# Kernel optimization log

Measured on AMD Instinct MI355X. Metric: run time of the kernel, lower is better.

The kernel has to match this reference:

```python
import jax, jax.numpy as jnp
import numpy as np


def setup_inputs() -> dict:
    key = jax.random.key(0)
    ks = jax.random.split(key, 6)
    B, S, D, H = 8, 1024, 1024, 16
    dk = D // H
    inputs = jax.random.normal(ks[0], (B, S, D), dtype=jnp.float32)
    mask = jnp.ones((B, S), dtype=jnp.float32)
    scale = 0.02
    W_q = jax.random.normal(ks[1], (H, D, dk), dtype=jnp.float32) * scale
    W_k = jax.random.normal(ks[2], (H, D, dk), dtype=jnp.float32) * scale
    W_v = jax.random.normal(ks[3], (D, D), dtype=jnp.float32) * scale
    W_o = jax.random.normal(ks[4], (D, D), dtype=jnp.float32) * scale
    return {"inputs": inputs, "mask": mask, "W_q": W_q, "W_k": W_k,
            "W_v": W_v, "W_o": W_o}


def reference(inputs, mask, W_q, W_k, W_v, W_o):
    B, S, D = inputs.shape
    H, _, dk = W_q.shape
    # combined causal + padding mask: 1.0 where attention is disallowed
    causal = 1.0 - jnp.tril(jnp.ones((S, S), dtype=jnp.float32))  # [S,S]
    input_mask = mask[:, None, :] * mask[:, :, None]              # [B,S,S]
    bad = jnp.maximum(causal[None, :, :], 1.0 - input_mask)       # [B,S,S]

    V = jnp.einsum('bsd,de->bse', inputs, W_v)                    # shared values
    Q = jnp.einsum('bsd,hdk->bhsk', inputs, W_q)
    K = jnp.einsum('bsd,hdk->bhsk', inputs, W_k)
    scores = jnp.einsum('bhqk,bhsk->bhqs', Q, K) / jnp.sqrt(jnp.float32(dk))
    scores = scores - bad[:, None, :, :] * 1e9
    attn = jax.nn.softmax(scores, axis=-1)                        # [B,H,S,S]
    attn_avg = jnp.mean(attn, axis=1)                             # [B,S,S]
    Hout = jnp.einsum('bqs,bse->bqe', attn_avg, V)
    output = jnp.einsum('bqe,ed->bqd', Hout, W_o)
    return (output, attn_avg)
```

## Files before the change

kernel.cpp:

```cpp
#include <hip/hip_runtime.h>

typedef unsigned short ushort;
typedef __bf16 bf16x8 __attribute__((ext_vector_type(8)));
typedef float f32x4 __attribute__((ext_vector_type(4)));
typedef unsigned short us8v __attribute__((ext_vector_type(8)));

__device__ __forceinline__ ushort f2bf(float f) {
  unsigned u = __builtin_bit_cast(unsigned, f);
  u += 0x7FFFu + ((u >> 16) & 1u);
  return (ushort)(u >> 16);
}

__device__ __forceinline__ bf16x8 ld_bf16x8(const ushort* p) {
  uint4 v = *(const uint4*)p;
  return __builtin_bit_cast(bf16x8, v);
}

__device__ __forceinline__ void gl16(const ushort* g, ushort* l) {
  __builtin_amdgcn_global_load_lds(
      (const __attribute__((address_space(1))) void*)g,
      (__attribute__((address_space(3))) void*)l, 16, 0, 0);
}

__global__ __launch_bounds__(256) void pack_x(const float* __restrict__ in,
                                              ushort* __restrict__ out) {
  long i = (long)blockIdx.x * 256 + threadIdx.x;
  const float4* s = (const float4*)in;
  float4 a = s[i * 2], b = s[i * 2 + 1];
  us8v o;
  o[0] = f2bf(a.x); o[1] = f2bf(a.y); o[2] = f2bf(a.z); o[3] = f2bf(a.w);
  o[4] = f2bf(b.x); o[5] = f2bf(b.y); o[6] = f2bf(b.z); o[7] = f2bf(b.w);
  *(us8v*)&out[i * 8] = o;
}

__global__ __launch_bounds__(256) void transpose_pack(
    const float* __restrict__ src, ushort* __restrict__ dst,
    int sC, int dLd, long sBatch, long dBatch, float scale) {
  src += (long)blockIdx.z * sBatch;
  dst += (long)blockIdx.z * dBatch;
  const int r0 = blockIdx.y * 64, c0 = blockIdx.x * 64;
  __shared__ ushort T[64 * 68];
  const int t = threadIdx.x;
#pragma unroll
  for (int i = 0; i < 4; ++i) {
    int ch = t + 256 * i;
    int r = ch >> 4, c4 = ch & 15;
    float4 v = *(const float4*)&src[(long)(r0 + r) * sC + c0 + c4 * 4];
    T[(c4 * 4 + 0) * 68 + r] = f2bf(v.x * scale);
    T[(c4 * 4 + 1) * 68 + r] = f2bf(v.y * scale);
    T[(c4 * 4 + 2) * 68 + r] = f2bf(v.z * scale);
    T[(c4 * 4 + 3) * 68 + r] = f2bf(v.w * scale);
  }
  __syncthreads();
#pragma unroll
  for (int i = 0; i < 4; ++i) {
    int ch = t + 256 * i;
    int c = ch >> 4, r4 = ch & 15;
    ushort4 o;
    o.x = T[c * 68 + r4 * 4 + 0];
    o.y = T[c * 68 + r4 * 4 + 1];
    o.z = T[c * 68 + r4 * 4 + 2];
    o.w = T[c * 68 + r4 * 4 + 3];
    *(ushort4*)&dst[(long)(c0 + c) * dLd + r0 + r4 * 4] = o;
  }
}

template <int EPI, bool CAUSAL, int BN>
__global__ __launch_bounds__(512, 2) void gemmS(
    const ushort* __restrict__ A, const ushort* __restrict__ Bt,
    int N, int K, long aB, long bB,
    ushort* __restrict__ O_q, ushort* __restrict__ O_k, ushort* __restrict__ O_v,
    ushort* __restrict__ O_b, long oB,
    float* __restrict__ O_f) {
  constexpr int NC = BN / 64;
  __shared__ __align__(16) ushort As[256 * 64];
  __shared__ __align__(16) ushort Bs[BN * 64];
  const int tid = threadIdx.x;
  const int lane = tid & 63, w = tid >> 6;
  const int lr = lane & 15, lg = lane >> 4;

  const int nx = gridDim.x, ny = gridDim.y;
  long nwg = (long)nx * ny * gridDim.z;
  long hwid = blockIdx.x + (long)nx * (blockIdx.y + (long)ny * blockIdx.z);
  long cpx = nwg >> 3;
  long sid = (hwid & 7) * cpx + (hwid >> 3);
  int bx = (int)(sid % nx);
  int t2 = (int)(sid / nx);
  int by = t2 % ny, z = t2 / ny;

  const int row0 = by * 256, col0 = bx * BN;
  A += (long)z * aB;
  Bt += (long)z * bB;
  const int wrow = (w >> 2) * 128;
  const int wcol = (w & 3) * (BN / 4);

  f32x4 acc[8][NC] = {};
  const int kmax = CAUSAL ? (K < row0 + 256 ? K : row0 + 256) : K;
  const int nk = kmax >> 6;

  for (int kt = 0; kt < nk; ++kt) {
    const int k0 = kt << 6;
    __syncthreads();
#pragma unroll
    for (int j = 0; j < 4; ++j) {
      int c = tid + 512 * j;
      int r = c >> 3, c8 = (c & 7) ^ (r & 7);
      gl16(&A[(long)(row0 + r) * K + k0 + c8 * 8], &As[c * 8]);
    }
#pragma unroll
    for (int j = 0; j < NC; ++j) {
      int c = tid + 512 * j;
      int r = c >> 3, c8 = (c & 7) ^ (r & 7);
      gl16(&Bt[(long)(col0 + r) * K + k0 + c8 * 8], &Bs[c * 8]);
    }
    __syncthreads();
#pragma unroll
    for (int kk = 0; kk < 2; ++kk) {
      bf16x8 bfr[NC];
#pragma unroll
      for (int n = 0; n < NC; ++n) {
        int row = wcol + n * 16 + lr;
        int c8 = (kk * 4 + lg) ^ (row & 7);
        bfr[n] = ld_bf16x8(&Bs[row * 64 + c8 * 8]);
      }
#pragma unroll
      for (int m = 0; m < 8; ++m) {
        int row = wrow + m * 16 + lr;
        int c8 = (kk * 4 + lg) ^ (row & 7);
        bf16x8 af = ld_bf16x8(&As[row * 64 + c8 * 8]);
#pragma unroll
        for (int n = 0; n < NC; ++n)
          acc[m][n] = __builtin_amdgcn_mfma_f32_16x16x32_bf16(af, bfr[n], acc[m][n], 0, 0, 0);
      }
    }
  }

#pragma unroll
  for (int m = 0; m < 8; ++m)
#pragma unroll
    for (int n = 0; n < NC; ++n)
#pragma unroll
      for (int r = 0; r < 4; ++r) {
        int gr = row0 + wrow + m * 16 + lg * 4 + r;
        int gc = col0 + wcol + n * 16 + lr;
        float v = acc[m][n][r];
        if (EPI == 0) {
          int b = gr >> 10, s = gr & 1023;
          if (gc < 1024) {
            int h = gc >> 6, kq = gc & 63;
            O_q[(((long)(b * 16 + h) << 10) + s) * 64 + kq] = f2bf(v);
          } else if (gc < 2048) {
            int n2 = gc - 1024;
            int h = n2 >> 6, kq = n2 & 63;
            O_k[(((long)(b * 16 + h) << 10) + s) * 64 + kq] = f2bf(v);
          } else {
            int e = gc - 2048;
            O_v[((long)(b << 10) + e) * 1024 + s] = f2bf(v);
          }
        } else if (EPI == 1) {
          (O_b + (long)z * oB)[(long)gr * N + gc] = f2bf(v);
        } else {
          O_f[(long)gr * N + gc] = v;
        }
      }
}

__global__ __launch_bounds__(512, 2) void attn16(
    const ushort* __restrict__ Qb, const ushort* __restrict__ Kb,
    const float* __restrict__ mask, float* __restrict__ attn_out,
    ushort* __restrict__ attnb) {
  __shared__ __align__(16) ushort Ks[2][4 * 128 * 64];
  __shared__ float redS[2][8][16];
  const int tid = threadIdx.x;
  const int lane = tid & 63, w = tid >> 6;
  const int lr = lane & 15, lg = lane >> 4;
  const int hw = blockIdx.x + 32 * blockIdx.y;
  const int b = hw & 7;
  const int x2 = hw >> 3;
  const int q0a = x2 * 16;
  const int q0b = (63 - x2) * 16;
  const int NTb = ((63 - x2) >> 3) + 1;
  const int n1 = (NTb - 4) << 10;
  const int NTWa = (x2 >> 4) * 2 + 2;
  const int NTWb = ((63 - x2) >> 4) * 2 + 2;

  float mqa[4], mqb[4], ms[8];
#pragma unroll
  for (int r = 0; r < 4; ++r) {
    mqa[r] = mask[b * 1024 + q0a + lg * 4 + r];
    mqb[r] = mask[b * 1024 + q0b + lg * 4 + r];
  }
#pragma unroll
  for (int t = 0; t < 8; ++t) ms[t] = mask[b * 1024 + t * 128 + w * 16 + lr];

  auto stageG = [&](int buf, int t0, int nch, int h) {
    const long hb = ((long)(b * 16 + h)) << 10;
#pragma unroll 2
    for (int i = tid; i < nch; i += 512) {
      int j = i >> 10, r = (i >> 3) & 127, c8 = i & 7;
      gl16(&Kb[(hb + (t0 + j) * 128 + r) * 64 + ((c8 ^ (r & 7)) << 3)],
           &Ks[buf][i * 8]);
    }
  };

  const int row = w * 16 + lr;
  const int cs0 = ((0 + lg) ^ (row & 7)) * 8;
  const int cs1 = ((4 + lg) ^ (row & 7)) * 8;

  stageG(0, 0, 4096, 0);
  __syncthreads();

  f32x4 acca[4] = {};
  f32x4 accb[8] = {};
#pragma unroll 1
  for (int h = 0; h < 16; ++h) {
    const long hb = ((long)(b * 16 + h)) << 10;
    const bf16x8 qa0 = ld_bf16x8(&Qb[(hb + q0a + lr) * 64 + lg * 8]);
    const bf16x8 qa1 = ld_bf16x8(&Qb[(hb + q0a + lr) * 64 + 32 + lg * 8]);
    const bf16x8 qb0 = ld_bf16x8(&Qb[(hb + q0b + lr) * 64 + lg * 8]);
    const bf16x8 qb1 = ld_bf16x8(&Qb[(hb + q0b + lr) * 64 + 32 + lg * 8]);

    stageG(1, 4, n1, h);

    f32x4 sca[4], scb[8];
    float psa[4] = {0.f, 0.f, 0.f, 0.f}, psb[4] = {0.f, 0.f, 0.f, 0.f};
#pragma unroll
    for (int t = 0; t < 4; ++t) {
      const int sb = t * 128 + w * 16;
      const ushort* kr = &Ks[0][(t * 128 + row) * 64];
      bf16x8 k0 = ld_bf16x8(kr + cs0);
      bf16x8 k1 = ld_bf16x8(kr + cs1);
      {
        f32x4 d = {};
        d = __builtin_amdgcn_mfma_f32_16x16x32_bf16(qb0, k0, d, 0, 0, 0);
        d = __builtin_amdgcn_mfma_f32_16x16x32_bf16(qb1, k1, d, 0, 0, 0);
#pragma unroll
        for (int r = 0; r < 4; ++r) {
          float e = __expf(d[r]) * (mqb[r] * ms[t]);
          scb[t][r] = e;
          psb[r] += e;
        }
      }
      if (sb <= q0a) {
        f32x4 d = {};
        d = __builtin_amdgcn_mfma_f32_16x16x32_bf16(qa0, k0, d, 0, 0, 0);
        d = __builtin_amdgcn_mfma_f32_16x16x32_bf16(qa1, k1, d, 0, 0, 0);
#pragma unroll
        for (int r = 0; r < 4; ++r) {
          float e = __expf(d[r]) * (mqa[r] * ms[t]);
          if (sb == q0a) e = (lr <= lg * 4 + r) ? e : 0.f;
          sca[t][r] = e;
          psa[r] += e;
        }
      }
    }
    __syncthreads();

    if (h < 15) stageG(0, 0, 4096, h + 1);

#pragma unroll
    for (int t = 4; t < 8; ++t) {
      const int sb = t * 128 + w * 16;
      if (sb <= q0b) {
        const ushort* kr = &Ks[1][((t - 4) * 128 + row) * 64];
        bf16x8 k0 = ld_bf16x8(kr + cs0);
        bf16x8 k1 = ld_bf16x8(kr + cs1);
        f32x4 d = {};
        d = __builtin_amdgcn_mfma_f32_16x16x32_bf16(qb0, k0, d, 0, 0, 0);
        d = __builtin_amdgcn_mfma_f32_16x16x32_bf16(qb1, k1, d, 0, 0, 0);
#pragma unroll
        for (int r = 0; r < 4; ++r) {
          float e = __expf(d[r]) * (mqb[r] * ms[t]);
          if (sb == q0b) e = (lr <= lg * 4 + r) ? e : 0.f;
          scb[t][r] = e;
          psb[r] += e;
        }
      }
    }
#pragma unroll
    for (int r = 0; r < 4; ++r) {
      psa[r] += __shfl_xor(psa[r], 1);
      psa[r] += __shfl_xor(psa[r], 2);
      psa[r] += __shfl_xor(psa[r], 4);
      psa[r] += __shfl_xor(psa[r], 8);
      psb[r] += __shfl_xor(psb[r], 1);
      psb[r] += __shfl_xor(psb[r], 2);
      psb[r] += __shfl_xor(psb[r], 4);
      psb[r] += __shfl_xor(psb[r], 8);
    }
    if (lr == 0) {
#pragma unroll
      for (int r = 0; r < 4; ++r) {
        redS[0][w][lg * 4 + r] = psa[r];
        redS[1][w][lg * 4 + r] = psb[r];
      }
    }
    __syncthreads();

#pragma unroll
    for (int r = 0; r < 4; ++r) {
      float ta = 0.f, tb = 0.f;
#pragma unroll
      for (int ww = 0; ww < 8; ++ww) {
        ta += redS[0][ww][lg * 4 + r];
        tb += redS[1][ww][lg * 4 + r];
      }
      float ra = __builtin_amdgcn_rcpf(ta);
      float rb = __builtin_amdgcn_rcpf(tb);
#pragma unroll
      for (int t = 0; t < 4; ++t) {
        const int sb = t * 128 + w * 16;
        if (sb <= q0a) acca[t][r] += sca[t][r] * ra;
      }
#pragma unroll
      for (int t = 0; t < 8; ++t) {
        const int sb = t * 128 + w * 16;
        if (sb <= q0b) accb[t][r] += scb[t][r] * rb;
      }
    }
  }

#pragma unroll
  for (int t = 0; t < 8; ++t) {
    int s = t * 128 + w * 16 + lr;
#pragma unroll
    for (int r = 0; r < 4; ++r) {
      {
        int q = q0a + lg * 4 + r;
        float v = (t < 4 ? acca[t][r] : 0.f) * 0.0625f;
        long o = ((long)(b * 1024 + q) << 10) + s;
        attn_out[o] = v;
        if (t < NTWa) attnb[o] = f2bf(v);
      }
      {
        int q = q0b + lg * 4 + r;
        float v = accb[t][r] * 0.0625f;
        long o = ((long)(b * 1024 + q) << 10) + s;
        attn_out[o] = v;
        if (t < NTWb) attnb[o] = f2bf(v);
      }
    }
  }
}

extern "C" void kernel_launch(void* const* d_in, const int* in_sizes, int n_in,
                              void* d_out, int out_size, void* d_ws, size_t ws_size,
                              hipStream_t stream) {
  const float* inputs = (const float*)d_in[0];
  const float* mask   = (const float*)d_in[1];
  const float* W_q    = (const float*)d_in[2];
  const float* W_k    = (const float*)d_in[3];
  const float* W_v    = (const float*)d_in[4];
  const float* W_o    = (const float*)d_in[5];
  float* out = (float*)d_out;

  ushort* Xb    = (ushort*)d_ws;
  ushort* WqkvT = Xb + 8192L * 1024;
  ushort* WoT   = WqkvT + 3072L * 1024;
  ushort* Qb    = WoT + 1024L * 1024;
  ushort* Kb    = Qb + 8L * 16 * 1024 * 64;
  ushort* Vt    = Kb + 8L * 16 * 1024 * 64;
  ushort* attnb = Vt + 8L * 1024 * 1024;
  ushort* Houtb = attnb + 8L * 1024 * 1024;

  pack_x<<<4096, 256, 0, stream>>>(inputs, Xb);
  transpose_pack<<<dim3(1, 16, 16), 256, 0, stream>>>(W_q, WqkvT, 64, 1024,
                                                      65536L, 64L * 1024, 0.125f);
  transpose_pack<<<dim3(1, 16, 16), 256, 0, stream>>>(W_k, WqkvT + 1024L * 1024, 64, 1024,
                                                      65536L, 64L * 1024, 1.0f);
  transpose_pack<<<dim3(16, 16, 1), 256, 0, stream>>>(W_v, WqkvT + 2048L * 1024, 1024, 1024,
                                                      0L, 0L, 1.0f);
  transpose_pack<<<dim3(16, 16, 1), 256, 0, stream>>>(W_o, WoT, 1024, 1024,
                                                      0L, 0L, 1.0f);
  gemmS<0, false, 192><<<dim3(16, 32, 1), 512, 0, stream>>>(
      Xb, WqkvT, 3072, 1024, 0L, 0L, Qb, Kb, Vt, nullptr, 0L, nullptr);
  attn16<<<dim3(32, 8), 512, 0, stream>>>(Qb, Kb, mask, out + 8388608L, attnb);
  gemmS<1, true, 128><<<dim3(8, 4, 8), 512, 0, stream>>>(
      attnb, Vt, 1024, 1024, 1048576L, 1048576L,
      nullptr, nullptr, nullptr, Houtb, 1048576L, nullptr);
  gemmS<2, false, 128><<<dim3(8, 32, 1), 512, 0, stream>>>(
      Houtb, WoT, 1024, 1024, 0L, 0L,
      nullptr, nullptr, nullptr, nullptr, 0L, out);
}
```

Baseline: 250.5 us.

## Switch GEMMs to 128x128 tiles with 256 threads and trim causal padding

Replaces the 256xBN, 512-thread GEMM with a 128x128-tile, 256-thread kernel. It uses a 2x2 wave layout with 4x4 MFMA fragments per wave and allows 3 blocks per CU. A template flag selects which grid index (rows or columns) varies fastest in the block-to-tile mapping. Because the causal attn@V GEMM now reads K only up to row0+128, attn16 writes fewer padding tiles, which cuts extra stores. The trade is more blocks and better load balance against less data reuse per tile, so global/LDS traffic per FLOP goes up.

```diff
diff --git a/kernel.cpp b/kernel.cpp
--- a/kernel.cpp
+++ b/kernel.cpp
@@ -65,16 +65,15 @@
   }
 }
 
-template <int EPI, bool CAUSAL, int BN>
-__global__ __launch_bounds__(512, 2) void gemmS(
+template <int EPI, bool CAUSAL, int SWZ>
+__global__ __launch_bounds__(256, 3) void gemm4(
     const ushort* __restrict__ A, const ushort* __restrict__ Bt,
     int N, int K, long aB, long bB,
     ushort* __restrict__ O_q, ushort* __restrict__ O_k, ushort* __restrict__ O_v,
     ushort* __restrict__ O_b, long oB,
     float* __restrict__ O_f) {
-  constexpr int NC = BN / 64;
-  __shared__ __align__(16) ushort As[256 * 64];
-  __shared__ __align__(16) ushort Bs[BN * 64];
+  __shared__ __align__(16) ushort As[128 * 64];
+  __shared__ __align__(16) ushort Bs[128 * 64];
   const int tid = threadIdx.x;
   const int lane = tid & 63, w = tid >> 6;
   const int lr = lane & 15, lg = lane >> 4;
@@ -84,18 +83,26 @@
   long hwid = blockIdx.x + (long)nx * (blockIdx.y + (long)ny * blockIdx.z);
   long cpx = nwg >> 3;
   long sid = (hwid & 7) * cpx + (hwid >> 3);
-  int bx = (int)(sid % nx);
-  int t2 = (int)(sid / nx);
-  int by = t2 % ny, z = t2 / ny;
-
-  const int row0 = by * 256, col0 = bx * BN;
+  int bx, by, z;
+  if (SWZ == 1) {
+    by = (int)(sid % ny);
+    int t2 = (int)(sid / ny);
+    bx = t2 % nx;
+    z = t2 / nx;
+  } else {
+    bx = (int)(sid % nx);
+    int t2 = (int)(sid / nx);
+    by = t2 % ny;
+    z = t2 / ny;
+  }
+
+  const int row0 = by * 128, col0 = bx * 128;
   A += (long)z * aB;
   Bt += (long)z * bB;
-  const int wrow = (w >> 2) * 128;
-  const int wcol = (w & 3) * (BN / 4);
-
-  f32x4 acc[8][NC] = {};
-  const int kmax = CAUSAL ? (K < row0 + 256 ? K : row0 + 256) : K;
+  const int wr = (w >> 1) * 64, wc = (w & 1) * 64;
+
+  f32x4 acc[4][4] = {};
+  const int kmax = CAUSAL ? (K < row0 + 128 ? K : row0 + 128) : K;
   const int nk = kmax >> 6;
 
   for (int kt = 0; kt < nk; ++kt) {
@@ -103,46 +110,43 @@
     __syncthreads();
 #pragma unroll
     for (int j = 0; j < 4; ++j) {
-      int c = tid + 512 * j;
+      int c = tid + 256 * j;
       int r = c >> 3, c8 = (c & 7) ^ (r & 7);
       gl16(&A[(long)(row0 + r) * K + k0 + c8 * 8], &As[c * 8]);
-    }
-#pragma unroll
-    for (int j = 0; j < NC; ++j) {
-      int c = tid + 512 * j;
-      int r = c >> 3, c8 = (c & 7) ^ (r & 7);
       gl16(&Bt[(long)(col0 + r) * K + k0 + c8 * 8], &Bs[c * 8]);
     }
     __syncthreads();
 #pragma unroll
     for (int kk = 0; kk < 2; ++kk) {
-      bf16x8 bfr[NC];
-#pragma unroll
-      for (int n = 0; n < NC; ++n) {
-        int row = wcol + n * 16 + lr;
+      bf16x8 af[4], bfr[4];
+#pragma unroll
+      for (int m = 0; m < 4; ++m) {
+        int row = wr + m * 16 + lr;
+        int c8 = (kk * 4 + lg) ^ (row & 7);
+        af[m] = ld_bf16x8(&As[row * 64 + c8 * 8]);
+      }
+#pragma unroll
+      for (int n = 0; n < 4; ++n) {
+        int row = wc + n * 16 + lr;
         int c8 = (kk * 4 + lg) ^ (row & 7);
         bfr[n] = ld_bf16x8(&Bs[row * 64 + c8 * 8]);
       }
 #pragma unroll
-      for (int m = 0; m < 8; ++m) {
-        int row = wrow + m * 16 + lr;
-        int c8 = (kk * 4 + lg) ^ (row & 7);
-        bf16x8 af = ld_bf16x8(&As[row * 64 + c8 * 8]);
-#pragma unroll
-        for (int n = 0; n < NC; ++n)
-          acc[m][n] = __builtin_amdgcn_mfma_f32_16x16x32_bf16(af, bfr[n], acc[m][n], 0, 0, 0);
-      }
-    }
-  }
-
-#pragma unroll
-  for (int m = 0; m < 8; ++m)
-#pragma unroll
-    for (int n = 0; n < NC; ++n)
+      for (int m = 0; m < 4; ++m)
+#pragma unroll
+        for (int n = 0; n < 4; ++n)
+          acc[m][n] = __builtin_amdgcn_mfma_f32_16x16x32_bf16(af[m], bfr[n], acc[m][n], 0, 0, 0);
+    }
+  }
+
+#pragma unroll
+  for (int m = 0; m < 4; ++m)
+#pragma unroll
+    for (int n = 0; n < 4; ++n)
 #pragma unroll
       for (int r = 0; r < 4; ++r) {
-        int gr = row0 + wrow + m * 16 + lg * 4 + r;
-        int gc = col0 + wcol + n * 16 + lr;
+        int gr = row0 + wr + m * 16 + lg * 4 + r;
+        int gc = col0 + wc + n * 16 + lr;
         float v = acc[m][n][r];
         if (EPI == 0) {
           int b = gr >> 10, s = gr & 1023;
@@ -181,8 +185,8 @@
   const int q0b = (63 - x2) * 16;
   const int NTb = ((63 - x2) >> 3) + 1;
   const int n1 = (NTb - 4) << 10;
-  const int NTWa = (x2 >> 4) * 2 + 2;
-  const int NTWb = ((63 - x2) >> 4) * 2 + 2;
+  const int NTWa = (x2 >> 3) + 1;
+  const int NTWb = ((63 - x2) >> 3) + 1;
 
   float mqa[4], mqb[4], ms[8];
 #pragma unroll
@@ -372,13 +376,13 @@
                                                       0L, 0L, 1.0f);
   transpose_pack<<<dim3(16, 16, 1), 256, 0, stream>>>(W_o, WoT, 1024, 1024,
                                                       0L, 0L, 1.0f);
-  gemmS<0, false, 192><<<dim3(16, 32, 1), 512, 0, stream>>>(
+  gemm4<0, false, 1><<<dim3(24, 64, 1), 256, 0, stream>>>(
       Xb, WqkvT, 3072, 1024, 0L, 0L, Qb, Kb, Vt, nullptr, 0L, nullptr);
   attn16<<<dim3(32, 8), 512, 0, stream>>>(Qb, Kb, mask, out + 8388608L, attnb);
-  gemmS<1, true, 128><<<dim3(8, 4, 8), 512, 0, stream>>>(
+  gemm4<1, true, 0><<<dim3(8, 8, 8), 256, 0, stream>>>(
       attnb, Vt, 1024, 1024, 1048576L, 1048576L,
       nullptr, nullptr, nullptr, Houtb, 1048576L, nullptr);
-  gemmS<2, false, 128><<<dim3(8, 32, 1), 512, 0, stream>>>(
+  gemm4<2, false, 1><<<dim3(8, 64, 1), 256, 0, stream>>>(
       Houtb, WoT, 1024, 1024, 0L, 0L,
       nullptr, nullptr, nullptr, nullptr, 0L, out);
 }
```

Result: no change. 248.0 us (-1.0%).
